# Optimization experiments

Measured on AMD Instinct MI355X. Metric: run time of the kernel, lower is better.

Reference implementation:

```python
import jax, jax.numpy as jnp
import numpy as np

N = 50000      # nodes
D = 64         # hidden size
E = 800000     # edges (avg degree 16)
DEPTH = 2      # GraphSAGE layers


def setup_inputs() -> dict:
    key = jax.random.key(0)
    k1, k2, k3, k4 = jax.random.split(key, 4)
    x = jax.random.normal(k1, (N, D), dtype=jnp.float32)
    edge_src = jax.random.randint(k2, (E,), 0, N)
    edge_dst = jax.random.randint(k3, (E,), 0, N)
    # per-layer weight applied to concat([h_self, h_neigh]) -> (D, 2D)
    W = jax.random.normal(k4, (DEPTH, D, 2 * D), dtype=jnp.float32) * (1.0 / np.sqrt(2 * D))
    return {"x": x, "W": W, "edge_src": edge_src, "edge_dst": edge_dst}


def reference(x, W, edge_src, edge_dst):
    n = x.shape[0]
    # neighbor counts for mean aggregation (isolated nodes -> 0 aggregate)
    deg = jax.ops.segment_sum(jnp.ones_like(edge_dst, dtype=x.dtype), edge_dst, num_segments=n)
    inv_deg = jnp.where(deg > 0, 1.0 / jnp.maximum(deg, 1.0), 0.0)  # [N]
    h = x
    for k in range(W.shape[0]):
        # mean of neighbor features: gather on src, scatter-add on dst
        neigh = jax.ops.segment_sum(h[edge_src], edge_dst, num_segments=n) * inv_deg[:, None]
        z = jnp.concatenate([h, neigh], axis=-1)          # [N, 2D]
        new = jax.nn.relu(jnp.einsum('nd,hd->nh', z, W[k]))  # W_k @ concat per node
        norm = jnp.linalg.norm(new, axis=-1, keepdims=True)
        h = new / jnp.maximum(norm, 1e-12)                 # L2 normalize per node
    return h
```

## Files before the change

kernel.cpp:

```cpp
#include <hip/hip_runtime.h>

#define HD 64

typedef short  bf16x8 __attribute__((ext_vector_type(8)));
typedef float  f32x4  __attribute__((ext_vector_type(4)));

__device__ inline float bf2f(ushort u) {
    unsigned x = ((unsigned)u) << 16;
    return __builtin_bit_cast(float, x);
}
__device__ inline ushort f2bf(float f) {
    unsigned u = __builtin_bit_cast(unsigned, f);
    u += 0x7fffu + ((u >> 16) & 1u);
    return (ushort)(u >> 16);
}

__global__ void zero_kernel(int4* __restrict__ p, int n4) {
    int i = blockIdx.x * blockDim.x + threadIdx.x;
    if (i < n4) p[i] = int4{0, 0, 0, 0};
}

__global__ void f2bf4_kernel(const float4* __restrict__ in, ushort4* __restrict__ ob, int n4) {
    int i = blockIdx.x * blockDim.x + threadIdx.x;
    if (i < n4) {
        float4 v = in[i];
        ushort4 o;
        o.x = f2bf(v.x); o.y = f2bf(v.y); o.z = f2bf(v.z); o.w = f2bf(v.w);
        ob[i] = o;
    }
}

__global__ void deg_part_kernel(const int* __restrict__ dst, int* __restrict__ deg,
                                int E, int N) {
    const int g = blockIdx.x & 7;
    const int per = (N + 7) / 8;
    const int lo = g * per;
    const int hi = min(N, lo + per);
    const int nb = gridDim.x >> 3;
    const int b = blockIdx.x >> 3;
    for (int e = b * blockDim.x + threadIdx.x; e < E; e += nb * blockDim.x) {
        int d = dst[e];
        if (d >= lo && d < hi) atomicAdd(&deg[d], 1);
    }
}

__global__ __launch_bounds__(1024) void scanA_kernel(const int* __restrict__ deg,
                                                     int* __restrict__ excl,
                                                     int* __restrict__ bsum, int N) {
    const int tid = threadIdx.x, lane = tid & 63, wid = tid >> 6;
    const int i = blockIdx.x * 1024 + tid;
    int v = (i < N) ? deg[i] : 0;
    int s = v;
#pragma unroll
    for (int off = 1; off < 64; off <<= 1) {
        int t = __shfl_up(s, off, 64);
        if (lane >= off) s += t;
    }
    __shared__ int wtot[16], woff[16];
    if (lane == 63) wtot[wid] = s;
    __syncthreads();
    if (wid == 0 && lane < 16) {
        int t = wtot[lane];
        int ss = t;
#pragma unroll
        for (int off = 1; off < 16; off <<= 1) {
            int u = __shfl_up(ss, off, 64);
            if (lane >= off) ss += u;
        }
        woff[lane] = ss - t;
        if (lane == 15) bsum[blockIdx.x] = ss;
    }
    __syncthreads();
    if (i < N) excl[i] = woff[wid] + (s - v);
}

__global__ __launch_bounds__(1024) void scanC_kernel(const int* __restrict__ excl,
                                                     const int* __restrict__ bsum,
                                                     const int* __restrict__ deg,
                                                     int* __restrict__ row_start,
                                                     int* __restrict__ cursor,
                                                     float* __restrict__ inv_deg,
                                                     int N, int E, int NB) {
    __shared__ int boff_s;
    const int tid = threadIdx.x;
    if (tid < 64) {
        int lane = tid;
        int v = (lane < NB) ? bsum[lane] : 0;
        int s = v;
#pragma unroll
        for (int off = 1; off < 64; off <<= 1) {
            int t = __shfl_up(s, off, 64);
            if (lane >= off) s += t;
        }
        if (lane == (int)blockIdx.x) boff_s = s - v;
    }
    __syncthreads();
    const int boff = boff_s;
    int i = blockIdx.x * 1024 + tid;
    if (i < N) {
        int e = excl[i] + boff;
        row_start[i] = e;
        cursor[i] = e;
        int d = deg[i];
        inv_deg[i] = (d > 0) ? 1.0f / (float)d : 0.0f;
    }
    if (blockIdx.x == 0 && tid == 0) row_start[N] = E;
}

__global__ void fill_part_kernel(const int* __restrict__ src, const int* __restrict__ dst,
                                 int* __restrict__ cursor, int* __restrict__ csr,
                                 int E, int N) {
    const int g = blockIdx.x & 7;
    const int per = (N + 7) / 8;
    const int lo = g * per;
    const int hi = min(N, lo + per);
    const int nb = gridDim.x >> 3;
    const int b = blockIdx.x >> 3;
    for (int e = b * blockDim.x + threadIdx.x; e < E; e += nb * blockDim.x) {
        int d = dst[e];
        if (d >= lo && d < hi) {
            int p = atomicAdd(&cursor[d], 1);
            csr[p] = src[e];
        }
    }
}

__global__ __launch_bounds__(256, 8) void agg_kernel(
    const ushort* __restrict__ hb, const int* __restrict__ row_start,
    const int* __restrict__ csr, const float* __restrict__ inv_deg,
    ushort* __restrict__ neighb, int N) {
    const int wv = (blockIdx.x * blockDim.x + threadIdx.x) >> 6;
    const int lane = threadIdx.x & 63;
    if (wv >= N) return;
    const int rs = row_start[wv];
    const int re = row_start[wv + 1];

    float a0 = 0.f, a1 = 0.f, a2 = 0.f, a3 = 0.f;
    float a4 = 0.f, a5 = 0.f, a6 = 0.f, a7 = 0.f;
    int j = rs;
    while (j < re) {
        int take = re - j;
        if (take > 64) take = 64;
        int idx = (lane < take) ? csr[j + lane] : 0;
        int i = 0;
        for (; i + 8 <= take; i += 8) {
            int s0 = __builtin_amdgcn_readlane(idx, i + 0);
            int s1 = __builtin_amdgcn_readlane(idx, i + 1);
            int s2 = __builtin_amdgcn_readlane(idx, i + 2);
            int s3 = __builtin_amdgcn_readlane(idx, i + 3);
            int s4 = __builtin_amdgcn_readlane(idx, i + 4);
            int s5 = __builtin_amdgcn_readlane(idx, i + 5);
            int s6 = __builtin_amdgcn_readlane(idx, i + 6);
            int s7 = __builtin_amdgcn_readlane(idx, i + 7);
            ushort v0 = hb[(long long)s0 * HD + lane];
            ushort v1 = hb[(long long)s1 * HD + lane];
            ushort v2 = hb[(long long)s2 * HD + lane];
            ushort v3 = hb[(long long)s3 * HD + lane];
            ushort v4 = hb[(long long)s4 * HD + lane];
            ushort v5 = hb[(long long)s5 * HD + lane];
            ushort v6 = hb[(long long)s6 * HD + lane];
            ushort v7 = hb[(long long)s7 * HD + lane];
            a0 += bf2f(v0); a1 += bf2f(v1); a2 += bf2f(v2); a3 += bf2f(v3);
            a4 += bf2f(v4); a5 += bf2f(v5); a6 += bf2f(v6); a7 += bf2f(v7);
        }
        for (; i < take; ++i) {
            int s0 = __builtin_amdgcn_readlane(idx, i);
            a0 += bf2f(hb[(long long)s0 * HD + lane]);
        }
        j += take;
    }
    float m = (((a0 + a1) + (a2 + a3)) + ((a4 + a5) + (a6 + a7))) * inv_deg[wv];
    neighb[(long long)wv * HD + lane] = f2bf(m);
}

__global__ __launch_bounds__(256) void gemm_mfma_kernel(
    const ushort* __restrict__ hb, const ushort* __restrict__ nbf,
    const ushort* __restrict__ Wb, float* __restrict__ out,
    ushort* __restrict__ hb_out, int N, int last) {
    const int lane = threadIdx.x & 63;
    const int w = threadIdx.x >> 6;
    const int base = blockIdx.x * 64 + w * 16;
    const int m = lane & 15;
    const int kq = lane >> 4;
    int anode = base + m;
    if (anode > N - 1) anode = N - 1;
    const long long arow = (long long)anode * HD;

    f32x4 acc[4] = {{0.f,0.f,0.f,0.f},{0.f,0.f,0.f,0.f},{0.f,0.f,0.f,0.f},{0.f,0.f,0.f,0.f}};
#pragma unroll
    for (int kk = 0; kk < 4; ++kk) {
        const ushort* ap = (kk < 2 ? hb : nbf) + arow + (kk & 1) * 32 + kq * 8;
        bf16x8 a = *(const bf16x8*)ap;
        const ushort* bp = Wb + (long long)m * 128 + kk * 32 + kq * 8;
#pragma unroll
        for (int t = 0; t < 4; ++t) {
            bf16x8 b = *(const bf16x8*)(bp + (long long)t * 16 * 128);
            acc[t] = __builtin_amdgcn_mfma_f32_16x16x32_bf16(a, b, acc[t], 0, 0, 0);
        }
    }

    float sq[4] = {0.f, 0.f, 0.f, 0.f};
#pragma unroll
    for (int t = 0; t < 4; ++t)
#pragma unroll
        for (int r = 0; r < 4; ++r) {
            float v = fmaxf(acc[t][r], 0.f);
            acc[t][r] = v;
            sq[r] += v * v;
        }
#pragma unroll
    for (int off = 1; off < 16; off <<= 1)
#pragma unroll
        for (int r = 0; r < 4; ++r) sq[r] += __shfl_xor(sq[r], off, 64);

    float scl[4];
#pragma unroll
    for (int r = 0; r < 4; ++r) scl[r] = 1.f / fmaxf(sqrtf(sq[r]), 1e-12f);

    if (last) {
#pragma unroll
        for (int r = 0; r < 4; ++r) {
            int node = base + kq * 4 + r;
            if (node < N) {
#pragma unroll
                for (int t = 0; t < 4; ++t)
                    out[(long long)node * HD + t * 16 + m] = acc[t][r] * scl[r];
            }
        }
    } else {
#pragma unroll
        for (int r = 0; r < 4; ++r) {
            int node = base + kq * 4 + r;
            if (node < N) {
#pragma unroll
                for (int t = 0; t < 4; ++t)
                    hb_out[(long long)node * HD + t * 16 + m] = f2bf(acc[t][r] * scl[r]);
            }
        }
    }
}

extern "C" void kernel_launch(void* const* d_in, const int* in_sizes, int n_in,
                              void* d_out, int out_size, void* d_ws, size_t ws_size,
                              hipStream_t stream) {
    const float* x    = (const float*)d_in[0];
    const float* W    = (const float*)d_in[1];
    const int*   esrc = (const int*)d_in[2];
    const int*   edst = (const int*)d_in[3];
    float* out = (float*)d_out;

    const int N = in_sizes[0] / HD;
    const int E = in_sizes[2];
    const int DEPTH = in_sizes[1] / (HD * 2 * HD);
    const int NB = (N + 1023) / 1024;

    auto align256 = [](size_t v) { return (v + 255) & ~(size_t)255; };
    char* ws = (char*)d_ws;
    int*    deg       = (int*)ws;     ws += align256((size_t)(N + 4) * 4);
    int*    excl      = (int*)ws;     ws += align256((size_t)N * 4);
    int*    bsum      = (int*)ws;     ws += align256(64 * 4);
    int*    row_start = (int*)ws;     ws += align256((size_t)(N + 1) * 4);
    int*    cursor    = (int*)ws;     ws += align256((size_t)N * 4);
    float*  inv_deg   = (float*)ws;   ws += align256((size_t)N * 4);
    int*    csr       = (int*)ws;     ws += align256((size_t)E * 4);
    ushort* hb0       = (ushort*)ws;  ws += align256((size_t)N * HD * 2);
    ushort* hb1       = (ushort*)ws;  ws += align256((size_t)N * HD * 2);
    ushort* neighb    = (ushort*)ws;  ws += align256((size_t)N * HD * 2);
    ushort* Wb        = (ushort*)ws;

    int n4 = (N + 3) / 4;
    zero_kernel<<<(n4 + 255) / 256, 256, 0, stream>>>((int4*)deg, n4);
    deg_part_kernel<<<2048, 256, 0, stream>>>(edst, deg, E, N);
    scanA_kernel<<<NB, 1024, 0, stream>>>(deg, excl, bsum, N);
    scanC_kernel<<<NB, 1024, 0, stream>>>(excl, bsum, deg, row_start, cursor, inv_deg, N, E, NB);
    fill_part_kernel<<<2048, 256, 0, stream>>>(esrc, edst, cursor, csr, E, N);

    int xn4 = N * HD / 4;
    f2bf4_kernel<<<(xn4 + 255) / 256, 256, 0, stream>>>((const float4*)x, (ushort4*)hb0, xn4);
    int wn4 = DEPTH * HD * 2 * HD / 4;
    f2bf4_kernel<<<(wn4 + 255) / 256, 256, 0, stream>>>((const float4*)W, (ushort4*)Wb, wn4);

    ushort* hb_cur = hb0;
    ushort* hb_nxt = hb1;
    for (int k = 0; k < DEPTH; ++k) {
        int last = (k == DEPTH - 1) ? 1 : 0;
        agg_kernel<<<(N * 64 + 255) / 256, 256, 0, stream>>>(hb_cur, row_start, csr,
                                                             inv_deg, neighb, N);
        gemm_mfma_kernel<<<(N + 63) / 64, 256, 0, stream>>>(hb_cur, neighb,
                                                            Wb + (size_t)k * HD * 2 * HD,
                                                            out, hb_nxt, N, last);
        ushort* t = hb_cur; hb_cur = hb_nxt; hb_nxt = t;
    }
}
```

Before: 173.5 us.

## Vectorize neighbor gather with 16-lane row groups and fuse prep kernels

The aggregation kernel now splits each wavefront into four 16-lane groups. Each lane loads 8 bytes (ushort4) of a neighbor row, so a wave works on 4–8 neighbor rows at once instead of one 2-byte element per lane per row, and the partial sums are combined across groups with xor shuffles at the end. This aims to cut the number of load instructions and raise memory-level parallelism in the gather. Separately, the degree zeroing and the two bf16 conversions are merged into one prep kernel to save two launches. The cost is extra shuffles and a final cross-group reduction.

```diff
diff --git a/kernel.cpp b/kernel.cpp
--- a/kernel.cpp
+++ b/kernel.cpp
@@ -15,19 +15,25 @@
     return (ushort)(u >> 16);
 }
 
-__global__ void zero_kernel(int4* __restrict__ p, int n4) {
+__global__ void prep_kernel(const float4* __restrict__ x, ushort4* __restrict__ hb, int xn4,
+                            const float4* __restrict__ W, ushort4* __restrict__ Wb, int wn4,
+                            int4* __restrict__ deg4, int dn4) {
     int i = blockIdx.x * blockDim.x + threadIdx.x;
-    if (i < n4) p[i] = int4{0, 0, 0, 0};
-}
-
-__global__ void f2bf4_kernel(const float4* __restrict__ in, ushort4* __restrict__ ob, int n4) {
-    int i = blockIdx.x * blockDim.x + threadIdx.x;
-    if (i < n4) {
-        float4 v = in[i];
-        ushort4 o;
-        o.x = f2bf(v.x); o.y = f2bf(v.y); o.z = f2bf(v.z); o.w = f2bf(v.w);
-        ob[i] = o;
-    }
+    if (i < xn4) {
+        float4 v = x[i];
+        ushort4 o; o.x = f2bf(v.x); o.y = f2bf(v.y); o.z = f2bf(v.z); o.w = f2bf(v.w);
+        hb[i] = o;
+        return;
+    }
+    int j = i - xn4;
+    if (j < wn4) {
+        float4 v = W[j];
+        ushort4 o; o.x = f2bf(v.x); o.y = f2bf(v.y); o.z = f2bf(v.z); o.w = f2bf(v.w);
+        Wb[j] = o;
+        return;
+    }
+    int k = j - wn4;
+    if (k < dn4) deg4[k] = int4{0, 0, 0, 0};
 }
 
 __global__ void deg_part_kernel(const int* __restrict__ dst, int* __restrict__ deg,
@@ -134,9 +140,11 @@
     if (wv >= N) return;
     const int rs = row_start[wv];
     const int re = row_start[wv + 1];
+    const int grp = lane >> 4;
+    const int sub = (lane & 15) << 2;
 
     float a0 = 0.f, a1 = 0.f, a2 = 0.f, a3 = 0.f;
-    float a4 = 0.f, a5 = 0.f, a6 = 0.f, a7 = 0.f;
+    float b0 = 0.f, b1 = 0.f, b2 = 0.f, b3 = 0.f;
     int j = rs;
     while (j < re) {
         int take = re - j;
@@ -144,33 +152,35 @@
         int idx = (lane < take) ? csr[j + lane] : 0;
         int i = 0;
         for (; i + 8 <= take; i += 8) {
-            int s0 = __builtin_amdgcn_readlane(idx, i + 0);
-            int s1 = __builtin_amdgcn_readlane(idx, i + 1);
-            int s2 = __builtin_amdgcn_readlane(idx, i + 2);
-            int s3 = __builtin_amdgcn_readlane(idx, i + 3);
-            int s4 = __builtin_amdgcn_readlane(idx, i + 4);
-            int s5 = __builtin_amdgcn_readlane(idx, i + 5);
-            int s6 = __builtin_amdgcn_readlane(idx, i + 6);
-            int s7 = __builtin_amdgcn_readlane(idx, i + 7);
-            ushort v0 = hb[(long long)s0 * HD + lane];
-            ushort v1 = hb[(long long)s1 * HD + lane];
-            ushort v2 = hb[(long long)s2 * HD + lane];
-            ushort v3 = hb[(long long)s3 * HD + lane];
-            ushort v4 = hb[(long long)s4 * HD + lane];
-            ushort v5 = hb[(long long)s5 * HD + lane];
-            ushort v6 = hb[(long long)s6 * HD + lane];
-            ushort v7 = hb[(long long)s7 * HD + lane];
-            a0 += bf2f(v0); a1 += bf2f(v1); a2 += bf2f(v2); a3 += bf2f(v3);
-            a4 += bf2f(v4); a5 += bf2f(v5); a6 += bf2f(v6); a7 += bf2f(v7);
-        }
-        for (; i < take; ++i) {
-            int s0 = __builtin_amdgcn_readlane(idx, i);
-            a0 += bf2f(hb[(long long)s0 * HD + lane]);
+            int s0 = __shfl(idx, i + grp, 64);
+            int s1 = __shfl(idx, i + 4 + grp, 64);
+            ushort4 v0 = *(const ushort4*)&hb[(long long)s0 * HD + sub];
+            ushort4 v1 = *(const ushort4*)&hb[(long long)s1 * HD + sub];
+            a0 += bf2f(v0.x); a1 += bf2f(v0.y); a2 += bf2f(v0.z); a3 += bf2f(v0.w);
+            b0 += bf2f(v1.x); b1 += bf2f(v1.y); b2 += bf2f(v1.z); b3 += bf2f(v1.w);
+        }
+        for (; i < take; i += 4) {
+            int p = i + grp;
+            int s = __shfl(idx, p < take ? p : 0, 64);
+            if (p < take) {
+                ushort4 v = *(const ushort4*)&hb[(long long)s * HD + sub];
+                a0 += bf2f(v.x); a1 += bf2f(v.y); a2 += bf2f(v.z); a3 += bf2f(v.w);
+            }
         }
         j += take;
     }
-    float m = (((a0 + a1) + (a2 + a3)) + ((a4 + a5) + (a6 + a7))) * inv_deg[wv];
-    neighb[(long long)wv * HD + lane] = f2bf(m);
+    a0 += b0; a1 += b1; a2 += b2; a3 += b3;
+    a0 += __shfl_xor(a0, 16, 64); a0 += __shfl_xor(a0, 32, 64);
+    a1 += __shfl_xor(a1, 16, 64); a1 += __shfl_xor(a1, 32, 64);
+    a2 += __shfl_xor(a2, 16, 64); a2 += __shfl_xor(a2, 32, 64);
+    a3 += __shfl_xor(a3, 16, 64); a3 += __shfl_xor(a3, 32, 64);
+    if (grp == 0) {
+        float inv = inv_deg[wv];
+        ushort4 o;
+        o.x = f2bf(a0 * inv); o.y = f2bf(a1 * inv);
+        o.z = f2bf(a2 * inv); o.w = f2bf(a3 * inv);
+        *(ushort4*)&neighb[(long long)wv * HD + sub] = o;
+    }
 }
 
 __global__ __launch_bounds__(256) void gemm_mfma_kernel(
@@ -256,7 +266,7 @@
 
     auto align256 = [](size_t v) { return (v + 255) & ~(size_t)255; };
     char* ws = (char*)d_ws;
-    int*    deg       = (int*)ws;     ws += align256((size_t)(N + 4) * 4);
+    int*    deg       = (int*)ws;     ws += align256((size_t)(N + 8) * 4);
     int*    excl      = (int*)ws;     ws += align256((size_t)N * 4);
     int*    bsum      = (int*)ws;     ws += align256(64 * 4);
     int*    row_start = (int*)ws;     ws += align256((size_t)(N + 1) * 4);
@@ -268,17 +278,19 @@
     ushort* neighb    = (ushort*)ws;  ws += align256((size_t)N * HD * 2);
     ushort* Wb        = (ushort*)ws;
 
-    int n4 = (N + 3) / 4;
-    zero_kernel<<<(n4 + 255) / 256, 256, 0, stream>>>((int4*)deg, n4);
+    int xn4 = N * HD / 4;
+    int wn4 = DEPTH * HD * 2 * HD / 4;
+    int dn4 = (N + 3) / 4;
+    int ptot = xn4 + wn4 + dn4;
+    prep_kernel<<<(ptot + 255) / 256, 256, 0, stream>>>(
+        (const float4*)x, (ushort4*)hb0, xn4,
+        (const float4*)W, (ushort4*)Wb, wn4,
+        (int4*)deg, dn4);
+
     deg_part_kernel<<<2048, 256, 0, stream>>>(edst, deg, E, N);
     scanA_kernel<<<NB, 1024, 0, stream>>>(deg, excl, bsum, N);
     scanC_kernel<<<NB, 1024, 0, stream>>>(excl, bsum, deg, row_start, cursor, inv_deg, N, E, NB);
     fill_part_kernel<<<2048, 256, 0, stream>>>(esrc, edst, cursor, csr, E, N);
-
-    int xn4 = N * HD / 4;
-    f2bf4_kernel<<<(xn4 + 255) / 256, 256, 0, stream>>>((const float4*)x, (ushort4*)hb0, xn4);
-    int wn4 = DEPTH * HD * 2 * HD / 4;
-    f2bf4_kernel<<<(wn4 + 255) / 256, 256, 0, stream>>>((const float4*)W, (ushort4*)Wb, wn4);
 
     ushort* hb_cur = hb0;
     ushort* hb_nxt = hb1;
```

After: 157.7 us. 1.1x faster.
